# Optimization experiments

Measured on AMD Instinct MI355X. Metric: run time of the kernel, lower is better.

## Reference

```python
import jax, jax.numpy as jnp
import numpy as np

SEQ_LEN = 131072
D_MODEL = 512
M = 1000
BETA = 0.5


def setup_inputs() -> dict:
    key = jax.random.key(0)
    k_t, k_m, k_wm, k_wt, k_bt = jax.random.split(key, 5)
    t = jax.random.normal(k_t, (SEQ_LEN,), dtype=jnp.float32)  # ~half negative -> masked
    marker = jax.random.randint(k_m, (SEQ_LEN,), 0, M, dtype=jnp.int32)
    W_m = jax.random.normal(k_wm, (D_MODEL, M), dtype=jnp.float32)
    W_t = jax.random.normal(k_wt, (D_MODEL,), dtype=jnp.float32)
    b_t = jax.random.normal(k_bt, (D_MODEL,), dtype=jnp.float32)
    return {"t": t, "marker": marker, "W_m": W_m, "W_t": W_t, "b_t": b_t}


def reference(t, marker, W_m, W_t, b_t):
    # one-hot matmul W_m @ one_hot(marker) == column gather of W_m -> row gather of W_m.T
    emb_m = jnp.take(W_m.T, marker, axis=0)            # [S, d_model]
    emb_t = t[:, None] * W_t[None, :] + b_t[None, :]   # [S, d_model]
    out = BETA * emb_m + (1.0 - BETA) * emb_t
    return jnp.where(t[:, None] < 0, jnp.zeros((), dtype=out.dtype), out)
```

## Files before the change

kernel.cpp:

```cpp
#include <hip/hip_runtime.h>

#define SEQ_LEN 131072
#define D_MODEL 512
#define M_SIZE  1000
#define BETA    0.5f

__global__ void transpose_wm_kernel(const float* __restrict__ W_m,
                                    float* __restrict__ W_mT) {
    __shared__ float tile[32][33];
    const int bx = blockIdx.x;
    const int by = blockIdx.y;
    const int tx = threadIdx.x;
    const int ty = threadIdx.y;

    const int m = bx * 32 + tx;
    const int d0 = by * 32;
    for (int i = ty; i < 32; i += 8) {
        const int d = d0 + i;
        tile[i][tx] = (m < M_SIZE) ? W_m[(long)d * M_SIZE + m] : 0.0f;
    }
    __syncthreads();
    const int m0 = bx * 32;
    for (int i = ty; i < 32; i += 8) {
        const int mm = m0 + i;
        if (mm < M_SIZE) W_mT[(long)mm * D_MODEL + d0 + tx] = tile[tx][i];
    }
}

__global__ void embed_kernel(const float* __restrict__ t,
                             const int* __restrict__ marker,
                             const float* __restrict__ W_mT,
                             const float* __restrict__ W_t,
                             const float* __restrict__ b_t,
                             float* __restrict__ out) {
    const long total4 = (long)SEQ_LEN * (D_MODEL / 4);
    const long stride = (long)gridDim.x * blockDim.x;
    for (long idx = (long)blockIdx.x * blockDim.x + threadIdx.x;
         idx < total4; idx += stride) {
        const int s = (int)(idx >> 7);
        const int c = (int)(idx & 127);
        const float tv = t[s];
        float4 o;
        if (tv < 0.0f) {
            o.x = 0.0f; o.y = 0.0f; o.z = 0.0f; o.w = 0.0f;
        } else {
            const int m = marker[s];
            const float4 em = reinterpret_cast<const float4*>(W_mT + (long)m * D_MODEL)[c];
            const float4 w  = reinterpret_cast<const float4*>(W_t)[c];
            const float4 b  = reinterpret_cast<const float4*>(b_t)[c];
            o.x = BETA * em.x + (1.0f - BETA) * fmaf(tv, w.x, b.x);
            o.y = BETA * em.y + (1.0f - BETA) * fmaf(tv, w.y, b.y);
            o.z = BETA * em.z + (1.0f - BETA) * fmaf(tv, w.z, b.z);
            o.w = BETA * em.w + (1.0f - BETA) * fmaf(tv, w.w, b.w);
        }
        reinterpret_cast<float4*>(out)[idx] = o;
    }
}

__global__ void embed_kernel_notrans(const float* __restrict__ t,
                                     const int* __restrict__ marker,
                                     const float* __restrict__ W_m,
                                     const float* __restrict__ W_t,
                                     const float* __restrict__ b_t,
                                     float* __restrict__ out) {
    const long total4 = (long)SEQ_LEN * (D_MODEL / 4);
    const long stride = (long)gridDim.x * blockDim.x;
    for (long idx = (long)blockIdx.x * blockDim.x + threadIdx.x;
         idx < total4; idx += stride) {
        const int s = (int)(idx >> 7);
        const int c = (int)(idx & 127);
        const float tv = t[s];
        float4 o;
        if (tv < 0.0f) {
            o.x = 0.0f; o.y = 0.0f; o.z = 0.0f; o.w = 0.0f;
        } else {
            const int m = marker[s];
            const int d = c * 4;
            const float4 w = reinterpret_cast<const float4*>(W_t)[c];
            const float4 b = reinterpret_cast<const float4*>(b_t)[c];
            o.x = BETA * W_m[(long)(d + 0) * M_SIZE + m] + (1.0f - BETA) * fmaf(tv, w.x, b.x);
            o.y = BETA * W_m[(long)(d + 1) * M_SIZE + m] + (1.0f - BETA) * fmaf(tv, w.y, b.y);
            o.z = BETA * W_m[(long)(d + 2) * M_SIZE + m] + (1.0f - BETA) * fmaf(tv, w.z, b.z);
            o.w = BETA * W_m[(long)(d + 3) * M_SIZE + m] + (1.0f - BETA) * fmaf(tv, w.w, b.w);
        }
        reinterpret_cast<float4*>(out)[idx] = o;
    }
}

extern "C" void kernel_launch(void* const* d_in, const int* in_sizes, int n_in,
                              void* d_out, int out_size, void* d_ws, size_t ws_size,
                              hipStream_t stream) {
    const float* t      = (const float*)d_in[0];
    const int*   marker = (const int*)d_in[1];
    const float* W_m    = (const float*)d_in[2];
    const float* W_t    = (const float*)d_in[3];
    const float* b_t    = (const float*)d_in[4];
    float* out = (float*)d_out;

    const size_t wmT_bytes = (size_t)M_SIZE * D_MODEL * sizeof(float);

    const int blocks = 2048;
    const int threads = 256;

    if (ws_size >= wmT_bytes) {
        float* W_mT = (float*)d_ws;
        dim3 tgrid((M_SIZE + 31) / 32, D_MODEL / 32);
        dim3 tblock(32, 8);
        transpose_wm_kernel<<<tgrid, tblock, 0, stream>>>(W_m, W_mT);
        embed_kernel<<<blocks, threads, 0, stream>>>(t, marker, W_mT, W_t, b_t, out);
    } else {
        embed_kernel_notrans<<<blocks, threads, 0, stream>>>(t, marker, W_m, W_t, b_t, out);
    }
}
```

Measured before the change: 56.78 us.

## Restructure embed kernel into row-strided loop with prefetch and nontemporal stores

The embedding kernel now assigns each 256-thread block two sequence rows per iteration and strides over rows. W_t and b_t are loaded once per thread, and t and marker for the next row are prefetched into registers. The 256 MB output is written with nontemporal stores so it does not evict cached W_mT rows. The fallback path without the transposed workspace is removed, so the code now assumes the workspace is large enough.

```diff
diff --git a/kernel.cpp b/kernel.cpp
--- a/kernel.cpp
+++ b/kernel.cpp
@@ -4,6 +4,8 @@
 #define D_MODEL 512
 #define M_SIZE  1000
 #define BETA    0.5f
+
+typedef float f32x4 __attribute__((ext_vector_type(4)));
 
 __global__ void transpose_wm_kernel(const float* __restrict__ W_m,
                                     float* __restrict__ W_mT) {
@@ -33,57 +35,44 @@
                              const float* __restrict__ W_t,
                              const float* __restrict__ b_t,
                              float* __restrict__ out) {
-    const long total4 = (long)SEQ_LEN * (D_MODEL / 4);
-    const long stride = (long)gridDim.x * blockDim.x;
-    for (long idx = (long)blockIdx.x * blockDim.x + threadIdx.x;
-         idx < total4; idx += stride) {
-        const int s = (int)(idx >> 7);
-        const int c = (int)(idx & 127);
-        const float tv = t[s];
-        float4 o;
+    const int c = threadIdx.x & 127;
+    const int rowInBlock = threadIdx.x >> 7;
+    const int sStride = (int)gridDim.x * 2;
+
+    const f32x4 w = reinterpret_cast<const f32x4*>(W_t)[c];
+    const f32x4 b = reinterpret_cast<const f32x4*>(b_t)[c];
+    f32x4* __restrict__ out4 = reinterpret_cast<f32x4*>(out);
+
+    int s = (int)blockIdx.x * 2 + rowInBlock;
+    if (s >= SEQ_LEN) return;
+
+    float tv = t[s];
+    int   m  = marker[s];
+
+    while (true) {
+        const int sn = s + sStride;
+        float tv_n = 0.0f;
+        int   m_n  = 0;
+        if (sn < SEQ_LEN) {
+            tv_n = t[sn];
+            m_n  = marker[sn];
+        }
+
+        f32x4 o;
         if (tv < 0.0f) {
-            o.x = 0.0f; o.y = 0.0f; o.z = 0.0f; o.w = 0.0f;
+            o = (f32x4)(0.0f);
         } else {
-            const int m = marker[s];
-            const float4 em = reinterpret_cast<const float4*>(W_mT + (long)m * D_MODEL)[c];
-            const float4 w  = reinterpret_cast<const float4*>(W_t)[c];
-            const float4 b  = reinterpret_cast<const float4*>(b_t)[c];
+            const f32x4 em =
+                reinterpret_cast<const f32x4*>(W_mT + (size_t)m * D_MODEL)[c];
             o.x = BETA * em.x + (1.0f - BETA) * fmaf(tv, w.x, b.x);
             o.y = BETA * em.y + (1.0f - BETA) * fmaf(tv, w.y, b.y);
             o.z = BETA * em.z + (1.0f - BETA) * fmaf(tv, w.z, b.z);
             o.w = BETA * em.w + (1.0f - BETA) * fmaf(tv, w.w, b.w);
         }
-        reinterpret_cast<float4*>(out)[idx] = o;
-    }
-}
+        __builtin_nontemporal_store(o, out4 + (size_t)s * (D_MODEL / 4) + c);
 
-__global__ void embed_kernel_notrans(const float* __restrict__ t,
-                                     const int* __restrict__ marker,
-                                     const float* __restrict__ W_m,
-                                     const float* __restrict__ W_t,
-                                     const float* __restrict__ b_t,
-                                     float* __restrict__ out) {
-    const long total4 = (long)SEQ_LEN * (D_MODEL / 4);
-    const long stride = (long)gridDim.x * blockDim.x;
-    for (long idx = (long)blockIdx.x * blockDim.x + threadIdx.x;
-         idx < total4; idx += stride) {
-        const int s = (int)(idx >> 7);
-        const int c = (int)(idx & 127);
-        const float tv = t[s];
-        float4 o;
-        if (tv < 0.0f) {
-            o.x = 0.0f; o.y = 0.0f; o.z = 0.0f; o.w = 0.0f;
-        } else {
-            const int m = marker[s];
-            const int d = c * 4;
-            const float4 w = reinterpret_cast<const float4*>(W_t)[c];
-            const float4 b = reinterpret_cast<const float4*>(b_t)[c];
-            o.x = BETA * W_m[(long)(d + 0) * M_SIZE + m] + (1.0f - BETA) * fmaf(tv, w.x, b.x);
-            o.y = BETA * W_m[(long)(d + 1) * M_SIZE + m] + (1.0f - BETA) * fmaf(tv, w.y, b.y);
-            o.z = BETA * W_m[(long)(d + 2) * M_SIZE + m] + (1.0f - BETA) * fmaf(tv, w.z, b.z);
-            o.w = BETA * W_m[(long)(d + 3) * M_SIZE + m] + (1.0f - BETA) * fmaf(tv, w.w, b.w);
-        }
-        reinterpret_cast<float4*>(out)[idx] = o;
+        if (sn >= SEQ_LEN) break;
+        s = sn; tv = tv_n; m = m_n;
     }
 }
 
@@ -97,18 +86,12 @@
     const float* b_t    = (const float*)d_in[4];
     float* out = (float*)d_out;
 
-    const size_t wmT_bytes = (size_t)M_SIZE * D_MODEL * sizeof(float);
+    float* W_mT = (float*)d_ws;
+    (void)ws_size;
 
-    const int blocks = 2048;
-    const int threads = 256;
+    dim3 tgrid((M_SIZE + 31) / 32, D_MODEL / 32);
+    dim3 tblock(32, 8);
+    transpose_wm_kernel<<<tgrid, tblock, 0, stream>>>(W_m, W_mT);
 
-    if (ws_size >= wmT_bytes) {
-        float* W_mT = (float*)d_ws;
-        dim3 tgrid((M_SIZE + 31) / 32, D_MODEL / 32);
-        dim3 tblock(32, 8);
-        transpose_wm_kernel<<<tgrid, tblock, 0, stream>>>(W_m, W_mT);
-        embed_kernel<<<blocks, threads, 0, stream>>>(t, marker, W_mT, W_t, b_t, out);
-    } else {
-        embed_kernel_notrans<<<blocks, threads, 0, stream>>>(t, marker, W_m, W_t, b_t, out);
-    }
+    embed_kernel<<<2048, 256, 0, stream>>>(t, marker, W_mT, W_t, b_t, out);
 }
```

After: 57.73 us. No clear change (+1.7%).

## Bucket unmasked rows by marker and write outputs per marker block

Applied to the files above, without the earlier changes.

Adds a bucketing pass that atomically groups unmasked sequence positions by marker. A main kernel then lets each block hold one W_mT row in registers and write all of that marker's output rows, while separate blocks write zeros for masked rows using nontemporal stores. This is meant to cut repeated gather traffic and fold beta and bias into a precomputed base and slope. In exchange it adds an extra kernel, atomics, scattered writes and a slow per-thread overflow path when a bucket exceeds its capacity.

```diff
diff --git a/kernel.cpp b/kernel.cpp
--- a/kernel.cpp
+++ b/kernel.cpp
@@ -4,35 +4,116 @@
 #define D_MODEL 512
 #define M_SIZE  1000
 #define BETA    0.5f
+#define CAP     192
+
+typedef float f32x4 __attribute__((ext_vector_type(4)));
+
+#define WMT_OFF 0
+#define CNT_OFF (2 * 1024 * 1024)
+#define BKT_OFF (CNT_OFF + 8192)
+#define WS_NEED (BKT_OFF + (size_t)M_SIZE * CAP * 8)
 
 __global__ void transpose_wm_kernel(const float* __restrict__ W_m,
-                                    float* __restrict__ W_mT) {
+                                    float* __restrict__ W_mT,
+                                    int* __restrict__ cnt) {
+    if (blockIdx.x == 0 && blockIdx.y == 0) {
+        const int tid = threadIdx.y * 32 + threadIdx.x;
+        for (int i = tid; i < M_SIZE; i += 256) cnt[i] = 0;
+    }
     __shared__ float tile[32][33];
-    const int bx = blockIdx.x;
-    const int by = blockIdx.y;
-    const int tx = threadIdx.x;
-    const int ty = threadIdx.y;
-
-    const int m = bx * 32 + tx;
-    const int d0 = by * 32;
+    const int tx = threadIdx.x, ty = threadIdx.y;
+    const int m = blockIdx.x * 32 + tx;
+    const int d0 = blockIdx.y * 32;
     for (int i = ty; i < 32; i += 8) {
-        const int d = d0 + i;
-        tile[i][tx] = (m < M_SIZE) ? W_m[(long)d * M_SIZE + m] : 0.0f;
+        tile[i][tx] = (m < M_SIZE) ? W_m[(long)(d0 + i) * M_SIZE + m] : 0.0f;
     }
     __syncthreads();
-    const int m0 = bx * 32;
+    const int m0 = blockIdx.x * 32;
     for (int i = ty; i < 32; i += 8) {
         const int mm = m0 + i;
         if (mm < M_SIZE) W_mT[(long)mm * D_MODEL + d0 + tx] = tile[tx][i];
     }
 }
 
-__global__ void embed_kernel(const float* __restrict__ t,
-                             const int* __restrict__ marker,
-                             const float* __restrict__ W_mT,
-                             const float* __restrict__ W_t,
-                             const float* __restrict__ b_t,
-                             float* __restrict__ out) {
+__global__ void bucket_kernel(const float* __restrict__ t,
+                              const int* __restrict__ marker,
+                              int* __restrict__ cnt,
+                              int2* __restrict__ bkt,
+                              const float* __restrict__ W_mT,
+                              const float* __restrict__ W_t,
+                              const float* __restrict__ b_t,
+                              float* __restrict__ out) {
+    const int s = blockIdx.x * 256 + threadIdx.x;
+    if (s >= SEQ_LEN) return;
+    const float tv = t[s];
+    if (tv < 0.0f) return;
+    const int m = marker[s];
+    const int pos = atomicAdd(&cnt[m], 1);
+    if (pos < CAP) {
+        int2 e; e.x = s; e.y = __float_as_int(tv);
+        bkt[m * CAP + pos] = e;
+    } else {
+        const float* em = W_mT + (size_t)m * D_MODEL;
+        for (int d = 0; d < D_MODEL; ++d)
+            out[(size_t)s * D_MODEL + d] =
+                BETA * em[d] + (1.0f - BETA) * fmaf(tv, W_t[d], b_t[d]);
+    }
+}
+
+#define NBKT_BLOCKS (M_SIZE * 2)
+#define NZ_BLOCKS   1024
+#define ZROWS       (SEQ_LEN / NZ_BLOCKS)
+
+__global__ __launch_bounds__(256) void
+embed_main(const float* __restrict__ t,
+           const int* __restrict__ cnt,
+           const int2* __restrict__ bkt,
+           const float* __restrict__ W_mT,
+           const float* __restrict__ W_t,
+           const float* __restrict__ b_t,
+           float* __restrict__ out) {
+    f32x4* __restrict__ out4 = reinterpret_cast<f32x4*>(out);
+
+    if (blockIdx.x < NBKT_BLOCKS) {
+        const int m = blockIdx.x >> 1;
+        const int h = blockIdx.x & 1;
+        const int c = threadIdx.x & 127;
+        const int r = threadIdx.x >> 7;
+
+        const f32x4 em = reinterpret_cast<const f32x4*>(W_mT + (size_t)m * D_MODEL)[c];
+        const f32x4 w  = reinterpret_cast<const f32x4*>(W_t)[c];
+        const f32x4 b  = reinterpret_cast<const f32x4*>(b_t)[c];
+        const f32x4 base  = BETA * em + (1.0f - BETA) * b;
+        const f32x4 slope = (1.0f - BETA) * w;
+
+        const int n = min(cnt[m], CAP);
+        const int2* __restrict__ bk = bkt + m * CAP;
+        for (int j = h * 2 + r; j < n; j += 4) {
+            const int2 e = bk[j];
+            const float tv = __int_as_float(e.y);
+            const f32x4 o = base + slope * tv;
+            __builtin_nontemporal_store(o, out4 + (size_t)e.x * (D_MODEL / 4) + c);
+        }
+    } else {
+        const int zb = (int)blockIdx.x - NBKT_BLOCKS;
+        const int c = threadIdx.x & 127;
+        const int rr = threadIdx.x >> 7;
+        const int s0 = zb * ZROWS;
+        const f32x4 z = (f32x4)(0.0f);
+        for (int i = 0; i < ZROWS; i += 2) {
+            const int s = s0 + i + rr;
+            if (t[s] < 0.0f)
+                __builtin_nontemporal_store(z, out4 + (size_t)s * (D_MODEL / 4) + c);
+        }
+    }
+}
+
+__global__ void embed_fallback(const float* __restrict__ t,
+                               const int* __restrict__ marker,
+                               const float* __restrict__ W_m,
+                               const float* __restrict__ W_t,
+                               const float* __restrict__ b_t,
+                               float* __restrict__ out) {
     const long total4 = (long)SEQ_LEN * (D_MODEL / 4);
     const long stride = (long)gridDim.x * blockDim.x;
     for (long idx = (long)blockIdx.x * blockDim.x + threadIdx.x;
@@ -40,50 +121,18 @@
         const int s = (int)(idx >> 7);
         const int c = (int)(idx & 127);
         const float tv = t[s];
-        float4 o;
-        if (tv < 0.0f) {
-            o.x = 0.0f; o.y = 0.0f; o.z = 0.0f; o.w = 0.0f;
-        } else {
-            const int m = marker[s];
-            const float4 em = reinterpret_cast<const float4*>(W_mT + (long)m * D_MODEL)[c];
-            const float4 w  = reinterpret_cast<const float4*>(W_t)[c];
-            const float4 b  = reinterpret_cast<const float4*>(b_t)[c];
-            o.x = BETA * em.x + (1.0f - BETA) * fmaf(tv, w.x, b.x);
-            o.y = BETA * em.y + (1.0f - BETA) * fmaf(tv, w.y, b.y);
-            o.z = BETA * em.z + (1.0f - BETA) * fmaf(tv, w.z, b.z);
-            o.w = BETA * em.w + (1.0f - BETA) * fmaf(tv, w.w, b.w);
-        }
-        reinterpret_cast<float4*>(out)[idx] = o;
-    }
-}
-
-__global__ void embed_kernel_notrans(const float* __restrict__ t,
-                                     const int* __restrict__ marker,
-                                     const float* __restrict__ W_m,
-                                     const float* __restrict__ W_t,
-                                     const float* __restrict__ b_t,
-                                     float* __restrict__ out) {
-    const long total4 = (long)SEQ_LEN * (D_MODEL / 4);
-    const long stride = (long)gridDim.x * blockDim.x;
-    for (long idx = (long)blockIdx.x * blockDim.x + threadIdx.x;
-         idx < total4; idx += stride) {
-        const int s = (int)(idx >> 7);
-        const int c = (int)(idx & 127);
-        const float tv = t[s];
-        float4 o;
-        if (tv < 0.0f) {
-            o.x = 0.0f; o.y = 0.0f; o.z = 0.0f; o.w = 0.0f;
-        } else {
+        f32x4 o = (f32x4)(0.0f);
+        if (tv >= 0.0f) {
             const int m = marker[s];
             const int d = c * 4;
-            const float4 w = reinterpret_cast<const float4*>(W_t)[c];
-            const float4 b = reinterpret_cast<const float4*>(b_t)[c];
+            const f32x4 w = reinterpret_cast<const f32x4*>(W_t)[c];
+            const f32x4 b = reinterpret_cast<const f32x4*>(b_t)[c];
             o.x = BETA * W_m[(long)(d + 0) * M_SIZE + m] + (1.0f - BETA) * fmaf(tv, w.x, b.x);
             o.y = BETA * W_m[(long)(d + 1) * M_SIZE + m] + (1.0f - BETA) * fmaf(tv, w.y, b.y);
             o.z = BETA * W_m[(long)(d + 2) * M_SIZE + m] + (1.0f - BETA) * fmaf(tv, w.z, b.z);
             o.w = BETA * W_m[(long)(d + 3) * M_SIZE + m] + (1.0f - BETA) * fmaf(tv, w.w, b.w);
         }
-        reinterpret_cast<float4*>(out)[idx] = o;
+        reinterpret_cast<f32x4*>(out)[idx] = o;
     }
 }
 
@@ -97,18 +146,23 @@
     const float* b_t    = (const float*)d_in[4];
     float* out = (float*)d_out;
 
-    const size_t wmT_bytes = (size_t)M_SIZE * D_MODEL * sizeof(float);
+    if (ws_size < WS_NEED) {
+        embed_fallback<<<2048, 256, 0, stream>>>(t, marker, W_m, W_t, b_t, out);
+        return;
+    }
 
-    const int blocks = 2048;
-    const int threads = 256;
+    char* ws = (char*)d_ws;
+    float* W_mT = (float*)(ws + WMT_OFF);
+    int*   cnt  = (int*)(ws + CNT_OFF);
+    int2*  bkt  = (int2*)(ws + BKT_OFF);
 
-    if (ws_size >= wmT_bytes) {
-        float* W_mT = (float*)d_ws;
-        dim3 tgrid((M_SIZE + 31) / 32, D_MODEL / 32);
-        dim3 tblock(32, 8);
-        transpose_wm_kernel<<<tgrid, tblock, 0, stream>>>(W_m, W_mT);
-        embed_kernel<<<blocks, threads, 0, stream>>>(t, marker, W_mT, W_t, b_t, out);
-    } else {
-        embed_kernel_notrans<<<blocks, threads, 0, stream>>>(t, marker, W_m, W_t, b_t, out);
-    }
+    dim3 tgrid((M_SIZE + 31) / 32, D_MODEL / 32);
+    dim3 tblock(32, 8);
+    transpose_wm_kernel<<<tgrid, tblock, 0, stream>>>(W_m, W_mT, cnt);
+
+    bucket_kernel<<<SEQ_LEN / 256, 256, 0, stream>>>(t, marker, cnt, bkt,
+                                                     W_mT, W_t, b_t, out);
+
+    embed_main<<<NBKT_BLOCKS + NZ_BLOCKS, 256, 0, stream>>>(t, cnt, bkt,
+                                                            W_mT, W_t, b_t, out);
 }
```

Measured after the change: 82.05 us. 44.5% more time.

## Store transposed embedding table in bf16 and use nontemporal output stores

Applied to the files above, without the earlier changes.

The transpose kernel now writes W_m transposed as bf16 (round-to-nearest-even), which halves the gathered table size and its read traffic. The main kernel keeps W_t and b_t in registers, gives each thread a fixed column across 32 rows, and writes output with nontemporal stores so the 256MB output stream does not evict the table from cache. Using bf16 for the embedding values adds rounding error on the gathered term.

```diff
diff --git a/kernel.cpp b/kernel.cpp
--- a/kernel.cpp
+++ b/kernel.cpp
@@ -5,34 +5,75 @@
 #define M_SIZE  1000
 #define BETA    0.5f
 
-__global__ void transpose_wm_kernel(const float* __restrict__ W_m,
-                                    float* __restrict__ W_mT) {
+typedef float f32x4 __attribute__((ext_vector_type(4)));
+typedef unsigned short u16x4 __attribute__((ext_vector_type(4)));
+
+__device__ inline unsigned short f32_to_bf16_rne(float f) {
+    unsigned int u = __float_as_uint(f);
+    u += 0x7fff + ((u >> 16) & 1);
+    return (unsigned short)(u >> 16);
+}
+
+__global__ void build_table_kernel(const float* __restrict__ W_m,
+                                   unsigned short* __restrict__ Tb) {
     __shared__ float tile[32][33];
-    const int bx = blockIdx.x;
-    const int by = blockIdx.y;
-    const int tx = threadIdx.x;
-    const int ty = threadIdx.y;
-
-    const int m = bx * 32 + tx;
-    const int d0 = by * 32;
+    const int tx = threadIdx.x, ty = threadIdx.y;
+    const int m = blockIdx.x * 32 + tx;
+    const int d0 = blockIdx.y * 32;
     for (int i = ty; i < 32; i += 8) {
-        const int d = d0 + i;
-        tile[i][tx] = (m < M_SIZE) ? W_m[(long)d * M_SIZE + m] : 0.0f;
+        tile[i][tx] = (m < M_SIZE) ? W_m[(long)(d0 + i) * M_SIZE + m] : 0.0f;
     }
     __syncthreads();
-    const int m0 = bx * 32;
+    const int m0 = blockIdx.x * 32;
     for (int i = ty; i < 32; i += 8) {
         const int mm = m0 + i;
-        if (mm < M_SIZE) W_mT[(long)mm * D_MODEL + d0 + tx] = tile[tx][i];
+        if (mm < M_SIZE)
+            Tb[(size_t)mm * D_MODEL + d0 + tx] = f32_to_bf16_rne(tile[tx][i]);
     }
 }
 
-__global__ void embed_kernel(const float* __restrict__ t,
-                             const int* __restrict__ marker,
-                             const float* __restrict__ W_mT,
-                             const float* __restrict__ W_t,
-                             const float* __restrict__ b_t,
-                             float* __restrict__ out) {
+__global__ __launch_bounds__(256) void
+embed_kernel(const float* __restrict__ t,
+             const int* __restrict__ marker,
+             const unsigned short* __restrict__ Tb,
+             const float* __restrict__ W_t,
+             const float* __restrict__ b_t,
+             float* __restrict__ out) {
+    const int c = threadIdx.x & 127;
+    const int r = threadIdx.x >> 7;
+    int s = (int)blockIdx.x * 2 + r;
+
+    const f32x4 w = reinterpret_cast<const f32x4*>(W_t)[c];
+    const f32x4 b = reinterpret_cast<const f32x4*>(b_t)[c];
+    f32x4* __restrict__ out4 = reinterpret_cast<f32x4*>(out);
+
+    for (int i = 0; i < 32; ++i, s += 4096) {
+        const float tv = t[s];
+        f32x4 o = (f32x4)(0.0f);
+        if (tv >= 0.0f) {
+            const int m = marker[s];
+            const u16x4 e = *reinterpret_cast<const u16x4*>(
+                Tb + (size_t)m * D_MODEL + c * 4);
+            f32x4 em;
+            em.x = __uint_as_float((unsigned)e.x << 16);
+            em.y = __uint_as_float((unsigned)e.y << 16);
+            em.z = __uint_as_float((unsigned)e.z << 16);
+            em.w = __uint_as_float((unsigned)e.w << 16);
+            o.x = BETA * em.x + (1.0f - BETA) * fmaf(tv, w.x, b.x);
+            o.y = BETA * em.y + (1.0f - BETA) * fmaf(tv, w.y, b.y);
+            o.z = BETA * em.z + (1.0f - BETA) * fmaf(tv, w.z, b.z);
+            o.w = BETA * em.w + (1.0f - BETA) * fmaf(tv, w.w, b.w);
+        }
+        __builtin_nontemporal_store(o, out4 + (size_t)s * (D_MODEL / 4) + c);
+    }
+}
+
+__global__ void embed_fallback(const float* __restrict__ t,
+                               const int* __restrict__ marker,
+                               const float* __restrict__ W_m,
+                               const float* __restrict__ W_t,
+                               const float* __restrict__ b_t,
+                               float* __restrict__ out) {
     const long total4 = (long)SEQ_LEN * (D_MODEL / 4);
     const long stride = (long)gridDim.x * blockDim.x;
     for (long idx = (long)blockIdx.x * blockDim.x + threadIdx.x;
@@ -40,50 +81,18 @@
         const int s = (int)(idx >> 7);
         const int c = (int)(idx & 127);
         const float tv = t[s];
-        float4 o;
-        if (tv < 0.0f) {
-            o.x = 0.0f; o.y = 0.0f; o.z = 0.0f; o.w = 0.0f;
-        } else {
-            const int m = marker[s];
-            const float4 em = reinterpret_cast<const float4*>(W_mT + (long)m * D_MODEL)[c];
-            const float4 w  = reinterpret_cast<const float4*>(W_t)[c];
-            const float4 b  = reinterpret_cast<const float4*>(b_t)[c];
-            o.x = BETA * em.x + (1.0f - BETA) * fmaf(tv, w.x, b.x);
-            o.y = BETA * em.y + (1.0f - BETA) * fmaf(tv, w.y, b.y);
-            o.z = BETA * em.z + (1.0f - BETA) * fmaf(tv, w.z, b.z);
-            o.w = BETA * em.w + (1.0f - BETA) * fmaf(tv, w.w, b.w);
-        }
-        reinterpret_cast<float4*>(out)[idx] = o;
-    }
-}
-
-__global__ void embed_kernel_notrans(const float* __restrict__ t,
-                                     const int* __restrict__ marker,
-                                     const float* __restrict__ W_m,
-                                     const float* __restrict__ W_t,
-                                     const float* __restrict__ b_t,
-                                     float* __restrict__ out) {
-    const long total4 = (long)SEQ_LEN * (D_MODEL / 4);
-    const long stride = (long)gridDim.x * blockDim.x;
-    for (long idx = (long)blockIdx.x * blockDim.x + threadIdx.x;
-         idx < total4; idx += stride) {
-        const int s = (int)(idx >> 7);
-        const int c = (int)(idx & 127);
-        const float tv = t[s];
-        float4 o;
-        if (tv < 0.0f) {
-            o.x = 0.0f; o.y = 0.0f; o.z = 0.0f; o.w = 0.0f;
-        } else {
+        f32x4 o = (f32x4)(0.0f);
+        if (tv >= 0.0f) {
             const int m = marker[s];
             const int d = c * 4;
-            const float4 w = reinterpret_cast<const float4*>(W_t)[c];
-            const float4 b = reinterpret_cast<const float4*>(b_t)[c];
+            const f32x4 w = reinterpret_cast<const f32x4*>(W_t)[c];
+            const f32x4 b = reinterpret_cast<const f32x4*>(b_t)[c];
             o.x = BETA * W_m[(long)(d + 0) * M_SIZE + m] + (1.0f - BETA) * fmaf(tv, w.x, b.x);
             o.y = BETA * W_m[(long)(d + 1) * M_SIZE + m] + (1.0f - BETA) * fmaf(tv, w.y, b.y);
             o.z = BETA * W_m[(long)(d + 2) * M_SIZE + m] + (1.0f - BETA) * fmaf(tv, w.z, b.z);
             o.w = BETA * W_m[(long)(d + 3) * M_SIZE + m] + (1.0f - BETA) * fmaf(tv, w.w, b.w);
         }
-        reinterpret_cast<float4*>(out)[idx] = o;
+        reinterpret_cast<f32x4*>(out)[idx] = o;
     }
 }
 
@@ -97,18 +106,16 @@
     const float* b_t    = (const float*)d_in[4];
     float* out = (float*)d_out;
 
-    const size_t wmT_bytes = (size_t)M_SIZE * D_MODEL * sizeof(float);
+    const size_t tb_bytes = (size_t)M_SIZE * D_MODEL * sizeof(unsigned short);
+    if (ws_size < tb_bytes) {
+        embed_fallback<<<2048, 256, 0, stream>>>(t, marker, W_m, W_t, b_t, out);
+        return;
+    }
 
-    const int blocks = 2048;
-    const int threads = 256;
+    unsigned short* Tb = (unsigned short*)d_ws;
+    dim3 tgrid((M_SIZE + 31) / 32, D_MODEL / 32);
+    dim3 tblock(32, 8);
+    build_table_kernel<<<tgrid, tblock, 0, stream>>>(W_m, Tb);
 
-    if (ws_size >= wmT_bytes) {
-        float* W_mT = (float*)d_ws;
-        dim3 tgrid((M_SIZE + 31) / 32, D_MODEL / 32);
-        dim3 tblock(32, 8);
-        transpose_wm_kernel<<<tgrid, tblock, 0, stream>>>(W_m, W_mT);
-        embed_kernel<<<blocks, threads, 0, stream>>>(t, marker, W_mT, W_t, b_t, out);
-    } else {
-        embed_kernel_notrans<<<blocks, threads, 0, stream>>>(t, marker, W_m, W_t, b_t, out);
-    }
+    embed_kernel<<<2048, 256, 0, stream>>>(t, marker, Tb, W_t, b_t, out);
 }
```

Result: slower. 59.44 us (+4.7%).
